# Performance work log

Hardware: AMD Instinct MI355X
Metric: run time of the kernel (lower is better)

The kernel has to match this reference:

```python
import jax, jax.numpy as jnp
import numpy as np
from jax import lax

K = 3
STRIDE = 1
PAD = 1


def setup_inputs() -> dict:
    key = jax.random.key(0)
    k1, k2, k3, k4 = jax.random.split(key, 4)
    B, C, H, W = 4, 64, 128, 128
    O = 64
    x = jax.random.normal(k1, (B, C, H, W), dtype=jnp.float32)
    weight = jax.random.normal(k2, (O, C, K, K), dtype=jnp.float32) * 0.05
    bias = jax.random.normal(k3, (O,), dtype=jnp.float32) * 0.05
    # original zero-inits offset_conv (degenerate); use small random weights instead
    offset_w = jax.random.normal(k4, (2 * K * K, C, 3, 3), dtype=jnp.float32) * 0.01
    offset_b = jnp.zeros((2 * K * K,), dtype=jnp.float32)
    return {"x": x, "weight": weight, "bias": bias, "offset_w": offset_w, "offset_b": offset_b}


def _deform_conv(x, weight, bias, offset_w, offset_b):
    B, C, H, W = x.shape
    O = weight.shape[0]
    K2 = K * K
    # offset predictor: 3x3 conv, pad 1, stride 1 -> [B, 2*K2, H, W]
    offsets = lax.conv_general_dilated(
        x, offset_w, window_strides=(1, 1), padding=[(1, 1), (1, 1)],
        dimension_numbers=("NCHW", "OIHW", "NCHW")) + offset_b[None, :, None, None]

    Ho = (H - K + 2 * PAD) // STRIDE + 1
    Wo = (W - K + 2 * PAD) // STRIDE + 1
    padded = jnp.pad(x, ((0, 0), (0, 0), (PAD, PAD), (PAD, PAD)))
    Hp, Wp = H + 2 * PAD, W + 2 * PAD

    off_h = offsets[:, :K2, :Ho, :Wo]   # [B,K2,Ho,Wo]
    off_w = offsets[:, K2:, :Ho, :Wo]

    # kernel tap grid, flattened row-major: idx = kh*K + kw
    grid_h = jnp.repeat(jnp.arange(K, dtype=x.dtype), K)   # [K2]
    grid_w = jnp.tile(jnp.arange(K, dtype=x.dtype), K)
    center_h = (jnp.arange(Ho, dtype=x.dtype) * STRIDE)
    center_w = (jnp.arange(Wo, dtype=x.dtype) * STRIDE)

    # sampling positions in padded coords, per original: grid + offset + center + PAD
    pos_h = grid_h[None, :, None, None] + off_h + center_h[None, None, :, None] + PAD
    pos_w = grid_w[None, :, None, None] + off_w + center_w[None, None, None, :] + PAD
    pos_h = jnp.clip(pos_h, 0.0, Hp - 1)
    pos_w = jnp.clip(pos_w, 0.0, Wp - 1)

    h0 = jnp.floor(pos_h).astype(jnp.int32)
    w0 = jnp.floor(pos_w).astype(jnp.int32)
    h1 = jnp.clip(h0 + 1, 0, Hp - 1)
    w1 = jnp.clip(w0 + 1, 0, Wp - 1)

    wh0 = h1.astype(x.dtype) - pos_h
    ww0 = w1.astype(x.dtype) - pos_w
    wh1 = pos_h - h0.astype(x.dtype)
    ww1 = pos_w - w0.astype(x.dtype)

    def gather(p, hi, wi):  # p:[C,Hp,Wp], hi/wi:[K2,Ho,Wo] -> [C,K2,Ho,Wo]
        return p[:, hi, wi]

    g = jax.vmap(gather)
    v00 = g(padded, h0, w0)
    v01 = g(padded, h0, w1)
    v10 = g(padded, h1, w0)
    v11 = g(padded, h1, w1)

    e = lambda a: a[:, None]  # [B,K2,Ho,Wo] -> [B,1,K2,Ho,Wo]
    val = (v00 * e(wh0 * ww0) + v01 * e(wh0 * ww1)
           + v10 * e(wh1 * ww0) + v11 * e(wh1 * ww1))  # [B,C,K2,Ho,Wo]

    out = jnp.einsum("bckhw,ock->bohw", val, weight.reshape(O, C, K2))
    return out + bias[None, :, None, None]


def reference(x, weight, bias, offset_w, offset_b):
    return _deform_conv(x, weight, bias, offset_w, offset_b)
```

## Files before the change

kernel.cpp:

```cpp
#include <hip/hip_runtime.h>

#define BB 4
#define CC 64
#define OO 64
#define HH 128
#define WW 128
#define HP 131
#define WP 132
#define HW (HH*WW)

#define TH 8
#define TW 8
#define WR 15
#define WC 15
#define NWIN (WR*WC)
#define PXS 36
#define NCHK (NWIN*9)
#define NCHK_PAD 2048

typedef __attribute__((ext_vector_type(8))) short short8;
typedef __attribute__((ext_vector_type(4))) float f32x4;

__device__ __forceinline__ unsigned f2b(float f) {
  unsigned u = __float_as_uint(f);
  return (u + 0x7fffu + ((u >> 16) & 1u)) >> 16;
}
__device__ __forceinline__ unsigned cvtpk(float lo, float hi) {
  unsigned r;
  asm("v_cvt_pk_bf16_f32 %0, %1, %2" : "=v"(r) : "v"(lo), "v"(hi));
  return r;
}
__device__ __forceinline__ float blo(unsigned r) { return __uint_as_float(r << 16); }
__device__ __forceinline__ float bhi(unsigned r) { return __uint_as_float(r & 0xffff0000u); }

__device__ __forceinline__ short8 lerp8(uint4 q00, uint4 q01, uint4 q10, uint4 q11,
                                        float w00, float w01, float w10, float w11) {
  unsigned c00[4] = {q00.x, q00.y, q00.z, q00.w};
  unsigned c01[4] = {q01.x, q01.y, q01.z, q01.w};
  unsigned c10[4] = {q10.x, q10.y, q10.z, q10.w};
  unsigned c11[4] = {q11.x, q11.y, q11.z, q11.w};
  union { unsigned u[4]; short8 v; } A;
#pragma unroll
  for (int t = 0; t < 4; ++t) {
    float lo = blo(c00[t]) * w00;
    lo = fmaf(blo(c01[t]), w01, lo);
    lo = fmaf(blo(c10[t]), w10, lo);
    lo = fmaf(blo(c11[t]), w11, lo);
    float hi = bhi(c00[t]) * w00;
    hi = fmaf(bhi(c01[t]), w01, hi);
    hi = fmaf(bhi(c10[t]), w10, hi);
    hi = fmaf(bhi(c11[t]), w11, hi);
    A.u[t] = cvtpk(lo, hi);
  }
  return A.v;
}

#define NROW (BB*HH)
#define NZB  12
#define NRPK 216

__global__ __launch_bounds__(256) void prep_kernel(const float* __restrict__ x,
                                                   const float* __restrict__ wt,
                                                   const float* __restrict__ ow,
                                                   unsigned* __restrict__ xp,
                                                   ushort* __restrict__ wbf,
                                                   ushort* __restrict__ owbf) {
  __shared__ float rbuf[64 * 129];
  int bid = blockIdx.x;
  int tid = threadIdx.x;

  if (bid < NROW) {
    int b = bid >> 7, h = bid & 127;
    const float* xs = x + ((size_t)b * CC * HH + h) * WW;
#pragma unroll
    for (int it = 0; it < 32; ++it) {
      int idx = it * 256 + tid;
      int c = idx >> 7, w = idx & 127;
      rbuf[c * 129 + w] = xs[(size_t)c * HW + w];
    }
    __syncthreads();
    int hp = h + 1;
    unsigned* xrow = xp + (size_t)b * (HP * WP * 32) + (size_t)hp * (WP * 32);
#pragma unroll
    for (int it = 0; it < 5; ++it) {
      int q = it * 256 + tid;
      if (q < WP * 8) {
        int wp = q >> 3, c8 = q & 7;
        uint4 v = make_uint4(0, 0, 0, 0);
        if (wp >= 1 && wp <= WW) {
          const float* rp = &rbuf[(c8 * 8) * 129 + (wp - 1)];
          v.x = cvtpk(rp[0], rp[129]);
          v.y = cvtpk(rp[2 * 129], rp[3 * 129]);
          v.z = cvtpk(rp[4 * 129], rp[5 * 129]);
          v.w = cvtpk(rp[6 * 129], rp[7 * 129]);
        }
        *(uint4*)(xrow + (size_t)wp * 32 + c8 * 4) = v;
      }
    }
  } else if (bid < NROW + NZB) {
    int z = bid - NROW;
    int b = z / 3, r = z % 3;
    int hp = (r == 0) ? 0 : ((r == 1) ? 129 : 130);
    unsigned* xrow = xp + (size_t)b * (HP * WP * 32) + (size_t)hp * (WP * 32);
    for (int q = tid; q < WP * 8; q += 256)
      *(uint4*)(xrow + (size_t)(q >> 3) * 32 + (q & 7) * 4) = make_uint4(0, 0, 0, 0);
  } else {
    int i = (bid - NROW - NZB) * 256 + tid;
    if (i < 72 * 512) {
      int j = i & 7, lane = (i >> 3) & 63, T = i >> 9;
      int nt = T & 3, sh = (T >> 2) & 1, kk = T >> 3;
      int o = nt * 16 + (lane & 15);
      int c = sh * 32 + (lane >> 4) * 8 + j;
      wbf[i] = (ushort)f2b(wt[(o * CC + c) * 9 + kk]);
    } else if (i < 72 * 512 + 36 * 512) {
      int i2 = i - 72 * 512;
      int j = i2 & 7, lane = (i2 >> 3) & 63, T = i2 >> 9;
      int nt = T & 1, sh = (T >> 1) & 1, kk = T >> 2;
      int oc = nt * 16 + (lane & 15);
      int c = sh * 32 + (lane >> 4) * 8 + j;
      owbf[i2] = (oc < 18) ? (ushort)f2b(ow[(oc * CC + c) * 9 + kk]) : (ushort)0;
    }
  }
}

__global__ __launch_bounds__(256, 4) void fused_deform(const unsigned* __restrict__ xp,
                                                       const ushort* __restrict__ wbf,
                                                       const ushort* __restrict__ owbf,
                                                       const float* __restrict__ obias,
                                                       const float* __restrict__ bias,
                                                       float* __restrict__ out) {
  __shared__ __align__(16) unsigned win[NCHK_PAD * 4];
  __shared__ __align__(16) float obuf[64 * 20];

  int tid = threadIdx.x;
  int blk0 = blockIdx.x;
  int xcd = blk0 & 7, i = blk0 >> 3;
  int s = xcd * 8 + (i >> 4);
  int b = s >> 4, ht = s & 15, wtile = i & 15;
  int H0 = ht * TH, W0 = wtile * TW;
  int rlo = H0 - 1, clo = W0 - 1;

  int wave = tid >> 6, lane = tid & 63, lm = lane & 15, lq = lane >> 4;
  const unsigned* xpb = xp + (size_t)b * (HP * WP * 32);

  {
#pragma unroll
    for (int it = 0; it < 8; ++it) {
      int q = it * 256 + tid;
      int qc = (q < NCHK) ? q : (NCHK - 1);
      int px = qc / 9, c = qc % 9;
      int cc = (c < 8) ? c : 0;
      int r = px / WC, cl = px % WC;
      int pr = rlo + r, pc = clo + cl;
      pr = min(max(pr, 0), HP - 1);
      pc = min(max(pc, 0), WP - 1);
      const unsigned* src = xpb + ((size_t)pr * WP + pc) * 32 + cc * 4;
      __builtin_amdgcn_global_load_lds(src, &win[(size_t)(it * 256 + wave * 64) * 4],
                                       16, 0, 0);
    }
  }
  __syncthreads();

  int row = 2 * wave + (lm >> 3);
  int col = lm & 7;
  int h = H0 + row, w = W0 + col;

  {
    f32x4 oacc0 = (f32x4)0.0f, oacc1 = (f32x4)0.0f;
#pragma unroll
    for (int kk = 0; kk < 9; ++kk) {
      const ushort* obp = owbf + (size_t)(kk * 4) * 512 + lane * 8;
      short8 ob00 = *(const short8*)(obp);
      short8 ob01 = *(const short8*)(obp + 512);
      short8 ob10 = *(const short8*)(obp + 1024);
      short8 ob11 = *(const short8*)(obp + 1536);
      int kh = kk / 3, kw = kk % 3;
      int widx = (row + kh + 1) * WC + (col + kw + 1);
      const unsigned* wp0 = &win[widx * PXS + lq * 4];
      short8 Ao0 = *(const short8*)wp0;
      short8 Ao1 = *(const short8*)(wp0 + 16);
      oacc0 = __builtin_amdgcn_mfma_f32_16x16x32_bf16(Ao0, ob00, oacc0, 0, 0, 0);
      oacc1 = __builtin_amdgcn_mfma_f32_16x16x32_bf16(Ao0, ob01, oacc1, 0, 0, 0);
      oacc0 = __builtin_amdgcn_mfma_f32_16x16x32_bf16(Ao1, ob10, oacc0, 0, 0, 0);
      oacc1 = __builtin_amdgcn_mfma_f32_16x16x32_bf16(Ao1, ob11, oacc1, 0, 0, 0);
    }
#pragma unroll
    for (int nt = 0; nt < 2; ++nt) {
      f32x4 oa = nt ? oacc1 : oacc0;
      int oc = nt * 16 + lm;
      if (oc < 18) {
        float bv = obias[oc];
        int idx = (oc < 9) ? (oc * 2) : ((oc - 9) * 2 + 1);
#pragma unroll
        for (int r2 = 0; r2 < 4; ++r2)
          obuf[(wave * 16 + lq * 4 + r2) * 20 + idx] = oa[r2] + bv;
      }
    }
  }
  __builtin_amdgcn_sched_barrier(0);

  float ph[9], pw[9];
  bool okall = true;
  {
    float orow[20];
    const float* orp = &obuf[(wave * 16 + lm) * 20];
#pragma unroll
    for (int q = 0; q < 5; ++q) *(float4*)&orow[q * 4] = *(const float4*)(orp + q * 4);
#pragma unroll
    for (int kk = 0; kk < 9; ++kk) {
      int kh = kk / 3, kw = kk % 3;
      float p_h = (((float)kh + orow[kk * 2]) + (float)h) + 1.0f;
      float p_w = (((float)kw + orow[kk * 2 + 1]) + (float)w) + 1.0f;
      p_h = fminf(fmaxf(p_h, 0.0f), 129.0f);
      p_w = fminf(fmaxf(p_w, 0.0f), 129.0f);
      ph[kk] = p_h;
      pw[kk] = p_w;
      int h0 = (int)floorf(p_h), w0 = (int)floorf(p_w);
      int wr0 = h0 - rlo, wc0 = w0 - clo;
      okall &= (wr0 >= 0) & (wr0 <= WR - 2) & (wc0 >= 0) & (wc0 <= WC - 2);
    }
  }

  f32x4 acc[4];
#pragma unroll
  for (int nt = 0; nt < 4; ++nt) acc[nt] = (f32x4)0.0f;

  if (__builtin_amdgcn_ballot_w64(okall) == ~0ull) {
#pragma unroll
    for (int kk = 0; kk < 9; ++kk) {
      const ushort* bp = wbf + (size_t)kk * 4096 + lane * 8;
      short8 b00 = *(const short8*)(bp);
      short8 b01 = *(const short8*)(bp + 512);
      short8 b02 = *(const short8*)(bp + 1024);
      short8 b03 = *(const short8*)(bp + 1536);
      short8 b10 = *(const short8*)(bp + 2048);
      short8 b11 = *(const short8*)(bp + 2560);
      short8 b12 = *(const short8*)(bp + 3072);
      short8 b13 = *(const short8*)(bp + 3584);

      float p_h = ph[kk], p_w = pw[kk];
      float fh0 = floorf(p_h), fw0 = floorf(p_w);
      int h0 = (int)fh0, w0 = (int)fw0;
      float wh1 = p_h - fh0, ww1 = p_w - fw0;
      float wh0 = 1.0f - wh1, ww0 = 1.0f - ww1;
      float w00 = wh0 * ww0, w01 = wh0 * ww1, w10 = wh1 * ww0, w11 = wh1 * ww1;
      const unsigned* pA = &win[((h0 - rlo) * WC + (w0 - clo)) * PXS + lq * 4];
      uint4 q00a = *(const uint4*)pA;
      uint4 q01a = *(const uint4*)(pA + PXS);
      uint4 q10a = *(const uint4*)(pA + WC * PXS);
      uint4 q11a = *(const uint4*)(pA + WC * PXS + PXS);
      uint4 q00b = *(const uint4*)(pA + 16);
      uint4 q01b = *(const uint4*)(pA + PXS + 16);
      uint4 q10b = *(const uint4*)(pA + WC * PXS + 16);
      uint4 q11b = *(const uint4*)(pA + WC * PXS + PXS + 16);
      short8 Af0 = lerp8(q00a, q01a, q10a, q11a, w00, w01, w10, w11);
      short8 Af1 = lerp8(q00b, q01b, q10b, q11b, w00, w01, w10, w11);

      acc[0] = __builtin_amdgcn_mfma_f32_16x16x32_bf16(Af0, b00, acc[0], 0, 0, 0);
      acc[1] = __builtin_amdgcn_mfma_f32_16x16x32_bf16(Af0, b01, acc[1], 0, 0, 0);
      acc[2] = __builtin_amdgcn_mfma_f32_16x16x32_bf16(Af0, b02, acc[2], 0, 0, 0);
      acc[3] = __builtin_amdgcn_mfma_f32_16x16x32_bf16(Af0, b03, acc[3], 0, 0, 0);
      acc[0] = __builtin_amdgcn_mfma_f32_16x16x32_bf16(Af1, b10, acc[0], 0, 0, 0);
      acc[1] = __builtin_amdgcn_mfma_f32_16x16x32_bf16(Af1, b11, acc[1], 0, 0, 0);
      acc[2] = __builtin_amdgcn_mfma_f32_16x16x32_bf16(Af1, b12, acc[2], 0, 0, 0);
      acc[3] = __builtin_amdgcn_mfma_f32_16x16x32_bf16(Af1, b13, acc[3], 0, 0, 0);
    }
  } else {
#pragma unroll
    for (int kk = 0; kk < 9; ++kk) {
      float p_h = ph[kk], p_w = pw[kk];
      float fh0 = floorf(p_h), fw0 = floorf(p_w);
      int h0 = (int)fh0, w0 = (int)fw0;
      float wh1 = p_h - fh0, ww1 = p_w - fw0;
      float wh0 = 1.0f - wh1, ww0 = 1.0f - ww1;
      float w00 = wh0 * ww0, w01 = wh0 * ww1, w10 = wh1 * ww0, w11 = wh1 * ww1;
      const unsigned* pG = xpb + ((size_t)h0 * WP + w0) * 32 + lq * 4;
      uint4 q00a = *(const uint4*)pG;
      uint4 q01a = *(const uint4*)(pG + 32);
      uint4 q10a = *(const uint4*)(pG + WP * 32);
      uint4 q11a = *(const uint4*)(pG + WP * 32 + 32);
      uint4 q00b = *(const uint4*)(pG + 16);
      uint4 q01b = *(const uint4*)(pG + 48);
      uint4 q10b = *(const uint4*)(pG + WP * 32 + 16);
      uint4 q11b = *(const uint4*)(pG + WP * 32 + 48);
      short8 A0v = lerp8(q00a, q01a, q10a, q11a, w00, w01, w10, w11);
      short8 A1v = lerp8(q00b, q01b, q10b, q11b, w00, w01, w10, w11);
      const ushort* bp = wbf + (size_t)kk * 4096 + lane * 8;
      acc[0] = __builtin_amdgcn_mfma_f32_16x16x32_bf16(A0v, *(const short8*)(bp), acc[0], 0, 0, 0);
      acc[1] = __builtin_amdgcn_mfma_f32_16x16x32_bf16(A0v, *(const short8*)(bp + 512), acc[1], 0, 0, 0);
      acc[2] = __builtin_amdgcn_mfma_f32_16x16x32_bf16(A0v, *(const short8*)(bp + 1024), acc[2], 0, 0, 0);
      acc[3] = __builtin_amdgcn_mfma_f32_16x16x32_bf16(A0v, *(const short8*)(bp + 1536), acc[3], 0, 0, 0);
      acc[0] = __builtin_amdgcn_mfma_f32_16x16x32_bf16(A1v, *(const short8*)(bp + 2048), acc[0], 0, 0, 0);
      acc[1] = __builtin_amdgcn_mfma_f32_16x16x32_bf16(A1v, *(const short8*)(bp + 2560), acc[1], 0, 0, 0);
      acc[2] = __builtin_amdgcn_mfma_f32_16x16x32_bf16(A1v, *(const short8*)(bp + 3072), acc[2], 0, 0, 0);
      acc[3] = __builtin_amdgcn_mfma_f32_16x16x32_bf16(A1v, *(const short8*)(bp + 3584), acc[3], 0, 0, 0);
    }
  }

  {
    int px0 = lq * 4;
    int hrow = H0 + 2 * wave + (px0 >> 3);
    int wcol = W0 + (px0 & 7);
#pragma unroll
    for (int nt = 0; nt < 4; ++nt) {
      int o = nt * 16 + lm;
      float bv = bias[o];
      float4 st = make_float4(acc[nt][0] + bv, acc[nt][1] + bv, acc[nt][2] + bv, acc[nt][3] + bv);
      *(float4*)(out + ((size_t)(b * OO + o) * HH + hrow) * WW + wcol) = st;
    }
  }
}

extern "C" void kernel_launch(void* const* d_in, const int* in_sizes, int n_in,
                              void* d_out, int out_size, void* d_ws, size_t ws_size,
                              hipStream_t stream) {
  const float* x        = (const float*)d_in[0];
  const float* weight   = (const float*)d_in[1];
  const float* bias     = (const float*)d_in[2];
  const float* offset_w = (const float*)d_in[3];
  const float* offset_b = (const float*)d_in[4];
  float* out = (float*)d_out;

  unsigned* xp  = (unsigned*)d_ws;
  ushort* wbf  = (ushort*)(xp + (size_t)BB * HP * WP * 32);
  ushort* owbf = wbf + (size_t)72 * 512;

  prep_kernel<<<NROW + NZB + NRPK, 256, 0, stream>>>(x, weight, offset_w, xp, wbf, owbf);
  fused_deform<<<1024, 256, 0, stream>>>(xp, wbf, owbf, offset_b, bias, out);
}
```

Before: 99.64 us.

## Drop LDS window staging; use single-wave blocks gathering directly from global

New measurement: 130.1 us. +30.6%, slower.

```diff
diff --git a/kernel.cpp b/kernel.cpp
--- a/kernel.cpp
+++ b/kernel.cpp
@@ -8,15 +8,6 @@
 #define HP 131
 #define WP 132
 #define HW (HH*WW)
-
-#define TH 8
-#define TW 8
-#define WR 15
-#define WC 15
-#define NWIN (WR*WC)
-#define PXS 36
-#define NCHK (NWIN*9)
-#define NCHK_PAD 2048
 
 typedef __attribute__((ext_vector_type(8))) short short8;
 typedef __attribute__((ext_vector_type(4))) float f32x4;
@@ -123,47 +114,23 @@
   }
 }
 
-__global__ __launch_bounds__(256, 4) void fused_deform(const unsigned* __restrict__ xp,
-                                                       const ushort* __restrict__ wbf,
-                                                       const ushort* __restrict__ owbf,
-                                                       const float* __restrict__ obias,
-                                                       const float* __restrict__ bias,
-                                                       float* __restrict__ out) {
-  __shared__ __align__(16) unsigned win[NCHK_PAD * 4];
-  __shared__ __align__(16) float obuf[64 * 20];
-
-  int tid = threadIdx.x;
+__global__ __launch_bounds__(64, 4) void fused_deform(const unsigned* __restrict__ xp,
+                                                      const ushort* __restrict__ wbf,
+                                                      const ushort* __restrict__ owbf,
+                                                      const float* __restrict__ obias,
+                                                      const float* __restrict__ bias,
+                                                      float* __restrict__ out) {
+  __shared__ __align__(16) float obuf[16 * 20];
+
+  int lane = threadIdx.x;
+  int lm = lane & 15, lq = lane >> 4;
   int blk0 = blockIdx.x;
-  int xcd = blk0 & 7, i = blk0 >> 3;
-  int s = xcd * 8 + (i >> 4);
-  int b = s >> 4, ht = s & 15, wtile = i & 15;
-  int H0 = ht * TH, W0 = wtile * TW;
-  int rlo = H0 - 1, clo = W0 - 1;
-
-  int wave = tid >> 6, lane = tid & 63, lm = lane & 15, lq = lane >> 4;
+  int work = (blk0 & 7) * 512 + (blk0 >> 3);
+  int b = work >> 10, rp = (work >> 4) & 63, wt = work & 15;
+  int row = lm >> 3;
+  int col = lm & 7;
+  int h = rp * 2 + row, w = wt * 8 + col;
   const unsigned* xpb = xp + (size_t)b * (HP * WP * 32);
-
-  {
-#pragma unroll
-    for (int it = 0; it < 8; ++it) {
-      int q = it * 256 + tid;
-      int qc = (q < NCHK) ? q : (NCHK - 1);
-      int px = qc / 9, c = qc % 9;
-      int cc = (c < 8) ? c : 0;
-      int r = px / WC, cl = px % WC;
-      int pr = rlo + r, pc = clo + cl;
-      pr = min(max(pr, 0), HP - 1);
-      pc = min(max(pc, 0), WP - 1);
-      const unsigned* src = xpb + ((size_t)pr * WP + pc) * 32 + cc * 4;
-      __builtin_amdgcn_global_load_lds(src, &win[(size_t)(it * 256 + wave * 64) * 4],
-                                       16, 0, 0);
-    }
-  }
-  __syncthreads();
-
-  int row = 2 * wave + (lm >> 3);
-  int col = lm & 7;
-  int h = H0 + row, w = W0 + col;
 
   {
     f32x4 oacc0 = (f32x4)0.0f, oacc1 = (f32x4)0.0f;
@@ -175,10 +142,9 @@
       short8 ob10 = *(const short8*)(obp + 1024);
       short8 ob11 = *(const short8*)(obp + 1536);
       int kh = kk / 3, kw = kk % 3;
-      int widx = (row + kh + 1) * WC + (col + kw + 1);
-      const unsigned* wp0 = &win[widx * PXS + lq * 4];
-      short8 Ao0 = *(const short8*)wp0;
-      short8 Ao1 = *(const short8*)(wp0 + 16);
+      const unsigned* pa = xpb + ((size_t)(h + kh) * WP + (w + kw)) * 32 + lq * 4;
+      short8 Ao0 = *(const short8*)pa;
+      short8 Ao1 = *(const short8*)(pa + 16);
       oacc0 = __builtin_amdgcn_mfma_f32_16x16x32_bf16(Ao0, ob00, oacc0, 0, 0, 0);
       oacc1 = __builtin_amdgcn_mfma_f32_16x16x32_bf16(Ao0, ob01, oacc1, 0, 0, 0);
       oacc0 = __builtin_amdgcn_mfma_f32_16x16x32_bf16(Ao1, ob10, oacc0, 0, 0, 0);
@@ -193,17 +159,16 @@
         int idx = (oc < 9) ? (oc * 2) : ((oc - 9) * 2 + 1);
 #pragma unroll
         for (int r2 = 0; r2 < 4; ++r2)
-          obuf[(wave * 16 + lq * 4 + r2) * 20 + idx] = oa[r2] + bv;
+          obuf[(lq * 4 + r2) * 20 + idx] = oa[r2] + bv;
       }
     }
   }
   __builtin_amdgcn_sched_barrier(0);
 
   float ph[9], pw[9];
-  bool okall = true;
   {
     float orow[20];
-    const float* orp = &obuf[(wave * 16 + lm) * 20];
+    const float* orp = &obuf[lm * 20];
 #pragma unroll
     for (int q = 0; q < 5; ++q) *(float4*)&orow[q * 4] = *(const float4*)(orp + q * 4);
 #pragma unroll
@@ -211,13 +176,8 @@
       int kh = kk / 3, kw = kk % 3;
       float p_h = (((float)kh + orow[kk * 2]) + (float)h) + 1.0f;
       float p_w = (((float)kw + orow[kk * 2 + 1]) + (float)w) + 1.0f;
-      p_h = fminf(fmaxf(p_h, 0.0f), 129.0f);
-      p_w = fminf(fmaxf(p_w, 0.0f), 129.0f);
-      ph[kk] = p_h;
-      pw[kk] = p_w;
-      int h0 = (int)floorf(p_h), w0 = (int)floorf(p_w);
-      int wr0 = h0 - rlo, wc0 = w0 - clo;
-      okall &= (wr0 >= 0) & (wr0 <= WR - 2) & (wc0 >= 0) & (wc0 <= WC - 2);
+      ph[kk] = fminf(fmaxf(p_h, 0.0f), 129.0f);
+      pw[kk] = fminf(fmaxf(p_w, 0.0f), 129.0f);
     }
   }
 
@@ -225,82 +185,50 @@
 #pragma unroll
   for (int nt = 0; nt < 4; ++nt) acc[nt] = (f32x4)0.0f;
 
-  if (__builtin_amdgcn_ballot_w64(okall) == ~0ull) {
-#pragma unroll
-    for (int kk = 0; kk < 9; ++kk) {
-      const ushort* bp = wbf + (size_t)kk * 4096 + lane * 8;
-      short8 b00 = *(const short8*)(bp);
-      short8 b01 = *(const short8*)(bp + 512);
-      short8 b02 = *(const short8*)(bp + 1024);
-      short8 b03 = *(const short8*)(bp + 1536);
-      short8 b10 = *(const short8*)(bp + 2048);
-      short8 b11 = *(const short8*)(bp + 2560);
-      short8 b12 = *(const short8*)(bp + 3072);
-      short8 b13 = *(const short8*)(bp + 3584);
-
-      float p_h = ph[kk], p_w = pw[kk];
-      float fh0 = floorf(p_h), fw0 = floorf(p_w);
-      int h0 = (int)fh0, w0 = (int)fw0;
-      float wh1 = p_h - fh0, ww1 = p_w - fw0;
-      float wh0 = 1.0f - wh1, ww0 = 1.0f - ww1;
-      float w00 = wh0 * ww0, w01 = wh0 * ww1, w10 = wh1 * ww0, w11 = wh1 * ww1;
-      const unsigned* pA = &win[((h0 - rlo) * WC + (w0 - clo)) * PXS + lq * 4];
-      uint4 q00a = *(const uint4*)pA;
-      uint4 q01a = *(const uint4*)(pA + PXS);
-      uint4 q10a = *(const uint4*)(pA + WC * PXS);
-      uint4 q11a = *(const uint4*)(pA + WC * PXS + PXS);
-      uint4 q00b = *(const uint4*)(pA + 16);
-      uint4 q01b = *(const uint4*)(pA + PXS + 16);
-      uint4 q10b = *(const uint4*)(pA + WC * PXS + 16);
-      uint4 q11b = *(const uint4*)(pA + WC * PXS + PXS + 16);
-      short8 Af0 = lerp8(q00a, q01a, q10a, q11a, w00, w01, w10, w11);
-      short8 Af1 = lerp8(q00b, q01b, q10b, q11b, w00, w01, w10, w11);
-
-      acc[0] = __builtin_amdgcn_mfma_f32_16x16x32_bf16(Af0, b00, acc[0], 0, 0, 0);
-      acc[1] = __builtin_amdgcn_mfma_f32_16x16x32_bf16(Af0, b01, acc[1], 0, 0, 0);
-      acc[2] = __builtin_amdgcn_mfma_f32_16x16x32_bf16(Af0, b02, acc[2], 0, 0, 0);
-      acc[3] = __builtin_amdgcn_mfma_f32_16x16x32_bf16(Af0, b03, acc[3], 0, 0, 0);
-      acc[0] = __builtin_amdgcn_mfma_f32_16x16x32_bf16(Af1, b10, acc[0], 0, 0, 0);
-      acc[1] = __builtin_amdgcn_mfma_f32_16x16x32_bf16(Af1, b11, acc[1], 0, 0, 0);
-      acc[2] = __builtin_amdgcn_mfma_f32_16x16x32_bf16(Af1, b12, acc[2], 0, 0, 0);
-      acc[3] = __builtin_amdgcn_mfma_f32_16x16x32_bf16(Af1, b13, acc[3], 0, 0, 0);
-    }
-  } else {
-#pragma unroll
-    for (int kk = 0; kk < 9; ++kk) {
-      float p_h = ph[kk], p_w = pw[kk];
-      float fh0 = floorf(p_h), fw0 = floorf(p_w);
-      int h0 = (int)fh0, w0 = (int)fw0;
-      float wh1 = p_h - fh0, ww1 = p_w - fw0;
-      float wh0 = 1.0f - wh1, ww0 = 1.0f - ww1;
-      float w00 = wh0 * ww0, w01 = wh0 * ww1, w10 = wh1 * ww0, w11 = wh1 * ww1;
-      const unsigned* pG = xpb + ((size_t)h0 * WP + w0) * 32 + lq * 4;
-      uint4 q00a = *(const uint4*)pG;
-      uint4 q01a = *(const uint4*)(pG + 32);
-      uint4 q10a = *(const uint4*)(pG + WP * 32);
-      uint4 q11a = *(const uint4*)(pG + WP * 32 + 32);
-      uint4 q00b = *(const uint4*)(pG + 16);
-      uint4 q01b = *(const uint4*)(pG + 48);
-      uint4 q10b = *(const uint4*)(pG + WP * 32 + 16);
-      uint4 q11b = *(const uint4*)(pG + WP * 32 + 48);
-      short8 A0v = lerp8(q00a, q01a, q10a, q11a, w00, w01, w10, w11);
-      short8 A1v = lerp8(q00b, q01b, q10b, q11b, w00, w01, w10, w11);
-      const ushort* bp = wbf + (size_t)kk * 4096 + lane * 8;
-      acc[0] = __builtin_amdgcn_mfma_f32_16x16x32_bf16(A0v, *(const short8*)(bp), acc[0], 0, 0, 0);
-      acc[1] = __builtin_amdgcn_mfma_f32_16x16x32_bf16(A0v, *(const short8*)(bp + 512), acc[1], 0, 0, 0);
-      acc[2] = __builtin_amdgcn_mfma_f32_16x16x32_bf16(A0v, *(const short8*)(bp + 1024), acc[2], 0, 0, 0);
-      acc[3] = __builtin_amdgcn_mfma_f32_16x16x32_bf16(A0v, *(const short8*)(bp + 1536), acc[3], 0, 0, 0);
-      acc[0] = __builtin_amdgcn_mfma_f32_16x16x32_bf16(A1v, *(const short8*)(bp + 2048), acc[0], 0, 0, 0);
-      acc[1] = __builtin_amdgcn_mfma_f32_16x16x32_bf16(A1v, *(const short8*)(bp + 2560), acc[1], 0, 0, 0);
-      acc[2] = __builtin_amdgcn_mfma_f32_16x16x32_bf16(A1v, *(const short8*)(bp + 3072), acc[2], 0, 0, 0);
-      acc[3] = __builtin_amdgcn_mfma_f32_16x16x32_bf16(A1v, *(const short8*)(bp + 3584), acc[3], 0, 0, 0);
-    }
+#pragma unroll
+  for (int kk = 0; kk < 9; ++kk) {
+    const ushort* bp = wbf + (size_t)kk * 4096 + lane * 8;
+    short8 b00 = *(const short8*)(bp);
+    short8 b01 = *(const short8*)(bp + 512);
+    short8 b02 = *(const short8*)(bp + 1024);
+    short8 b03 = *(const short8*)(bp + 1536);
+    short8 b10 = *(const short8*)(bp + 2048);
+    short8 b11 = *(const short8*)(bp + 2560);
+    short8 b12 = *(const short8*)(bp + 3072);
+    short8 b13 = *(const short8*)(bp + 3584);
+
+    float p_h = ph[kk], p_w = pw[kk];
+    float fh0 = floorf(p_h), fw0 = floorf(p_w);
+    int h0 = (int)fh0, w0 = (int)fw0;
+    float wh1 = p_h - fh0, ww1 = p_w - fw0;
+    float wh0 = 1.0f - wh1, ww0 = 1.0f - ww1;
+    float w00 = wh0 * ww0, w01 = wh0 * ww1, w10 = wh1 * ww0, w11 = wh1 * ww1;
+    const unsigned* pG = xpb + ((size_t)h0 * WP + w0) * 32 + lq * 4;
+    uint4 q00a = *(const uint4*)pG;
+    uint4 q01a = *(const uint4*)(pG + 32);
+    uint4 q10a = *(const uint4*)(pG + WP * 32);
+    uint4 q11a = *(const uint4*)(pG + WP * 32 + 32);
+    uint4 q00b = *(const uint4*)(pG + 16);
+    uint4 q01b = *(const uint4*)(pG + 48);
+    uint4 q10b = *(const uint4*)(pG + WP * 32 + 16);
+    uint4 q11b = *(const uint4*)(pG + WP * 32 + 48);
+    short8 A0v = lerp8(q00a, q01a, q10a, q11a, w00, w01, w10, w11);
+    short8 A1v = lerp8(q00b, q01b, q10b, q11b, w00, w01, w10, w11);
+
+    acc[0] = __builtin_amdgcn_mfma_f32_16x16x32_bf16(A0v, b00, acc[0], 0, 0, 0);
+    acc[1] = __builtin_amdgcn_mfma_f32_16x16x32_bf16(A0v, b01, acc[1], 0, 0, 0);
+    acc[2] = __builtin_amdgcn_mfma_f32_16x16x32_bf16(A0v, b02, acc[2], 0, 0, 0);
+    acc[3] = __builtin_amdgcn_mfma_f32_16x16x32_bf16(A0v, b03, acc[3], 0, 0, 0);
+    acc[0] = __builtin_amdgcn_mfma_f32_16x16x32_bf16(A1v, b10, acc[0], 0, 0, 0);
+    acc[1] = __builtin_amdgcn_mfma_f32_16x16x32_bf16(A1v, b11, acc[1], 0, 0, 0);
+    acc[2] = __builtin_amdgcn_mfma_f32_16x16x32_bf16(A1v, b12, acc[2], 0, 0, 0);
+    acc[3] = __builtin_amdgcn_mfma_f32_16x16x32_bf16(A1v, b13, acc[3], 0, 0, 0);
   }
 
   {
     int px0 = lq * 4;
-    int hrow = H0 + 2 * wave + (px0 >> 3);
-    int wcol = W0 + (px0 & 7);
+    int hrow = rp * 2 + (px0 >> 3);
+    int wcol = wt * 8 + (px0 & 7);
 #pragma unroll
     for (int nt = 0; nt < 4; ++nt) {
       int o = nt * 16 + lm;
@@ -326,5 +254,5 @@
   ushort* owbf = wbf + (size_t)72 * 512;
 
   prep_kernel<<<NROW + NZB + NRPK, 256, 0, stream>>>(x, weight, offset_w, xp, wbf, owbf);
-  fused_deform<<<1024, 256, 0, stream>>>(xp, wbf, owbf, offset_b, bias, out);
-}
+  fused_deform<<<4096, 64, 0, stream>>>(xp, wbf, owbf, offset_b, bias, out);
+}
```
